# Performance work log

Hardware: AMD Instinct MI355X
Metric: run time of the kernel (lower is better)

Reference implementation:

```python
import jax, jax.numpy as jnp
import numpy as np


def _pyramid(x2, k):
    # AdaptiveAvgPool2d(k) with H,W divisible by k == block mean, then nearest upsample back
    B, C, H, W = x2.shape
    p = x2.reshape(B, C, k, H // k, k, W // k).mean(axis=(3, 5))  # [B,C,k,k]
    return jnp.repeat(jnp.repeat(p, H // k, axis=2), W // k, axis=3)  # [B,C,H,W]


def setup_inputs() -> dict:
    key = jax.random.key(0)
    ks = jax.random.split(key, 8)
    B, C, H, W = 32, 256, 32, 32
    x1 = jax.random.normal(ks[0], (B, C, H, W), jnp.float32)
    x2 = jax.random.normal(ks[1], (B, C, H, W), jnp.float32)
    # 1x1 conv weights (kaiming-ish scale), stored as [out,in]
    Wq = jax.random.normal(ks[2], (C // 2, C), jnp.float32) * (1.0 / np.sqrt(C))
    bq = jnp.zeros((C // 2,), jnp.float32)
    Wk = jax.random.normal(ks[3], (C // 2, 4 * C), jnp.float32) * (1.0 / np.sqrt(4 * C))
    bk = jnp.zeros((C // 2,), jnp.float32)
    Wv = jax.random.normal(ks[4], (C, C), jnp.float32) * (1.0 / np.sqrt(C))
    bv = jnp.zeros((C,), jnp.float32)
    return {"x1": x1, "x2": x2, "Wq": Wq, "bq": bq, "Wk": Wk, "bk": bk, "Wv": Wv, "bv": bv}


def reference(x1, x2, Wq, bq, Wk, bk, Wv, bv):
    B, C, H, W = x1.shape
    HW = H * W
    # pyramid pool at scales 1,2,4, upsampled and concatenated with x2 -> [B,4C,H,W]
    x2p = jnp.concatenate([x2] + [_pyramid(x2, k) for k in (1, 2, 4)], axis=1)
    # 1x1 convs as channel contractions
    q = (jnp.einsum('oc,bchw->bohw', Wq, x1) + bq[None, :, None, None]).reshape(B, C // 2, HW)
    k = (jnp.einsum('oc,bchw->bohw', Wk, x2p) + bk[None, :, None, None]).reshape(B, C // 2, HW)
    v = (jnp.einsum('oc,bchw->bohw', Wv, x2) + bv[None, :, None, None]).reshape(B, C, HW)
    query = q.transpose(0, 2, 1)                         # [B,HW,C/2]
    attn = jax.nn.softmax(jnp.einsum('bic,bcj->bij', query, k), axis=-1)  # [B,HW,HW]
    out = jnp.einsum('bcj,bij->bci', v, attn).reshape(B, C, H, W)
    return out + x1
```

## Files before the change

kernel.cpp:

```cpp
#include <hip/hip_runtime.h>


typedef __attribute__((ext_vector_type(8))) short short8;
typedef __attribute__((ext_vector_type(4))) float f32x4;

#define MFMA(a, b, c) __builtin_amdgcn_mfma_f32_16x16x32_bf16((a), (b), (c), 0, 0, 0)

#define GLOAD16(gp, lp)                                                        \
    __builtin_amdgcn_global_load_lds(                                          \
        (const __attribute__((address_space(1))) unsigned int*)(gp),           \
        (__attribute__((address_space(3))) unsigned int*)(lp), 16, 0, 0)

__device__ __forceinline__ unsigned short f2bf(float f) {
    unsigned u = __builtin_bit_cast(unsigned, f);
    u = (u + 0x7FFFu + ((u >> 16) & 1u)) >> 16;
    return (unsigned short)u;
}

__device__ __forceinline__ short8 ld8(const unsigned short* p) {
    return *reinterpret_cast<const short8*>(p);
}
__device__ __forceinline__ short8 ld8b(const void* base, int byte_off) {
    return *reinterpret_cast<const short8*>((const char*)base + byte_off);
}

__global__ __launch_bounds__(256) void wconv_kernel(const float* Wq, const float* Wk,
                                                    const float* Wv,
                                                    unsigned short* wqb, unsigned short* wkb,
                                                    unsigned short* wvb) {
    int i = blockIdx.x * 256 + threadIdx.x;
    if (i < 32768) { wqb[i] = f2bf(Wq[i]); return; }
    if (i < 163840) { wkb[i - 32768] = f2bf(Wk[i - 32768]); return; }
    wvb[i - 163840] = f2bf(Wv[i - 163840]);
}

__global__ __launch_bounds__(256) void transpose_kernel(const float* __restrict__ x,
                                                        unsigned short* __restrict__ xt) {
    __shared__ unsigned short tile[64][65];
    int b = blockIdx.z, c0 = blockIdx.y * 64, n0 = blockIdx.x * 64;
    const float* src = x + ((size_t)b * 256 + c0) * 1024 + n0;
    int tid = threadIdx.x;
#pragma unroll
    for (int it = 0; it < 16; ++it) {
        int idx = it * 256 + tid;
        int cl = idx >> 6, nl = idx & 63;
        tile[cl][nl] = f2bf(src[(size_t)cl * 1024 + nl]);
    }
    __syncthreads();
    int nl = tid >> 2, cs = (tid & 3) * 16;
    unsigned short buf[16];
#pragma unroll
    for (int j = 0; j < 16; ++j) buf[j] = tile[cs + j][nl];
    unsigned int w[8];
#pragma unroll
    for (int k = 0; k < 8; ++k) w[k] = (unsigned)buf[2 * k] | ((unsigned)buf[2 * k + 1] << 16);
    unsigned short* dst = xt + ((size_t)b * 1024 + n0 + nl) * 256 + c0 + cs;
    uint4 u0; u0.x = w[0]; u0.y = w[1]; u0.z = w[2]; u0.w = w[3];
    uint4 u1; u1.x = w[4]; u1.y = w[5]; u1.z = w[6]; u1.w = w[7];
    reinterpret_cast<uint4*>(dst)[0] = u0;
    reinterpret_cast<uint4*>(dst)[1] = u1;
}

__global__ __launch_bounds__(64) void pool_kernel(const float* __restrict__ x2,
                                                  float* __restrict__ p1,
                                                  float* __restrict__ p2,
                                                  float* __restrict__ p4) {
    int bc = blockIdx.x;
    int t = threadIdx.x;
    const float* src = x2 + (size_t)bc * 1024;
    int dh = t >> 3, dw = t & 7;
    float s[16];
#pragma unroll
    for (int r = 0; r < 16; ++r)
        s[r] = src[((r >> 2) * 8 + dh) * 32 + (r & 3) * 8 + dw];
#pragma unroll
    for (int r = 0; r < 16; ++r) {
        float v = s[r];
        v += __shfl_xor(v, 1);  v += __shfl_xor(v, 2);  v += __shfl_xor(v, 4);
        v += __shfl_xor(v, 8);  v += __shfl_xor(v, 16); v += __shfl_xor(v, 32);
        s[r] = v;
    }
    if (t == 0) {
        float sq[4];
#pragma unroll
        for (int j = 0; j < 4; ++j) {
            int jh = j >> 1, jw = j & 1;
            sq[j] = s[8 * jh + 2 * jw] + s[8 * jh + 2 * jw + 1] +
                    s[8 * jh + 4 + 2 * jw] + s[8 * jh + 4 + 2 * jw + 1];
            p2[(size_t)bc * 4 + j] = sq[j] * (1.f / 256.f);
        }
#pragma unroll
        for (int r = 0; r < 16; ++r) p4[(size_t)bc * 16 + r] = s[r] * (1.f / 64.f);
        p1[bc] = (sq[0] + sq[1] + sq[2] + sq[3]) * (1.f / 1024.f);
    }
}

__global__ __launch_bounds__(256) void kadd_kernel(const float* __restrict__ Wk,
                                                   const float* __restrict__ bk,
                                                   const float* __restrict__ p1,
                                                   const float* __restrict__ p2,
                                                   const float* __restrict__ p4,
                                                   float* __restrict__ kadd) {
    int b = blockIdx.x >> 7, o = blockIdx.x & 127;
    int tid = threadIdx.x;
    const float* wr = Wk + (size_t)o * 1024;
    int c = tid;
    size_t bc = (size_t)b * 256 + c;
    float vals[21];
    vals[0] = wr[256 + c] * p1[bc];
    float w2 = wr[512 + c], w4 = wr[768 + c];
#pragma unroll
    for (int j = 0; j < 4; ++j) vals[1 + j] = w2 * p2[bc * 4 + j];
#pragma unroll
    for (int r = 0; r < 16; ++r) vals[5 + r] = w4 * p4[bc * 16 + r];

    int lane = tid & 63, wid = tid >> 6;
    __shared__ float red[21][4];
    __shared__ float tot[21];
#pragma unroll
    for (int k = 0; k < 21; ++k) {
        float v = vals[k];
        v += __shfl_xor(v, 1);  v += __shfl_xor(v, 2);  v += __shfl_xor(v, 4);
        v += __shfl_xor(v, 8);  v += __shfl_xor(v, 16); v += __shfl_xor(v, 32);
        if (lane == 0) red[k][wid] = v;
    }
    __syncthreads();
    if (tid < 21) tot[tid] = red[tid][0] + red[tid][1] + red[tid][2] + red[tid][3];
    __syncthreads();
    if (tid < 16) {
        int r = tid;
        int rr = ((r >> 2) >> 1) * 2 + ((r & 3) >> 1);
        kadd[((size_t)(b * 128 + o)) * 16 + r] = bk[o] + tot[0] + tot[1 + rr] + tot[5 + r];
    }
}

template <int MODE>
__global__ __launch_bounds__(256) void gemm_kernel(const unsigned short* __restrict__ A0,
                                                   const unsigned short* __restrict__ B0,
                                                   unsigned short* __restrict__ out0,
                                                   const float* __restrict__ bias,
                                                   const float* __restrict__ kadd) {
    int b = blockIdx.z;
    const unsigned short* A;
    const unsigned short* Bp;
    unsigned short* out;
    int lda, ldb, ldo;
    if (MODE == 0) { A = A0 + (size_t)b * 262144; lda = 256; Bp = B0; ldb = 256;  out = out0 + (size_t)b * 131072; ldo = 128; }
    if (MODE == 1) { A = A0 + (size_t)b * 262144; lda = 256; Bp = B0; ldb = 1024; out = out0 + (size_t)b * 131072; ldo = 128; }
    if (MODE == 2) { A = A0;                      lda = 256; Bp = B0 + (size_t)b * 262144; ldb = 256; out = out0 + (size_t)b * 262144; ldo = 1024; }

    __shared__ unsigned short alds[128 * 64];
    __shared__ unsigned short blds[128 * 64];

    int tid = threadIdx.x;
    int w = tid >> 6, lane = tid & 63;
    int lrow = lane & 15, lk8 = (lane >> 4) * 8;
    int lk16b = lk8 * 2;
    int swl = (lrow & 7) << 4;
    int row0 = blockIdx.x * 128;
    int col0 = blockIdx.y * 128;
    int wr = (w >> 1) * 64, wc = (w & 1) * 64;

    int soff = w * 1024 + (lane << 4);
    int srow = soff >> 7;
    int scol = ((soff & 127) ^ ((srow & 7) << 4)) >> 1;

    f32x4 z = {0.f, 0.f, 0.f, 0.f};
    f32x4 acc[4][4];
#pragma unroll
    for (int i = 0; i < 4; ++i)
#pragma unroll
        for (int j = 0; j < 4; ++j) acc[i][j] = z;

    for (int kc = 0; kc < 256; kc += 64) {
#pragma unroll
        for (int it = 0; it < 4; ++it) {
            int row = it * 32 + srow;
            GLOAD16(A + (size_t)(row0 + row) * lda + kc + scol,
                    (char*)alds + it * 4096 + w * 1024);
            GLOAD16(Bp + (size_t)(col0 + row) * ldb + kc + scol,
                    (char*)blds + it * 4096 + w * 1024);
        }
        asm volatile("s_waitcnt vmcnt(0)" ::: "memory");
        __syncthreads();

#pragma unroll
        for (int kh = 0; kh < 2; ++kh) {
            short8 af[4], bfr[4];
#pragma unroll
            for (int i = 0; i < 4; ++i)
                af[i] = ld8b(alds, ((wr + i * 16 + lrow) << 7) + (((kh << 6) + lk16b) ^ swl));
#pragma unroll
            for (int j = 0; j < 4; ++j)
                bfr[j] = ld8b(blds, ((wc + j * 16 + lrow) << 7) + (((kh << 6) + lk16b) ^ swl));
#pragma unroll
            for (int i = 0; i < 4; ++i)
#pragma unroll
                for (int j = 0; j < 4; ++j) acc[i][j] = MFMA(af[i], bfr[j], acc[i][j]);
        }
        __syncthreads();
    }

#pragma unroll
    for (int i = 0; i < 4; ++i) {
#pragma unroll
        for (int j = 0; j < 4; ++j) {
            int col = col0 + wc + j * 16 + lrow;
#pragma unroll
            for (int r = 0; r < 4; ++r) {
                int row = row0 + wr + i * 16 + (lane >> 4) * 4 + r;
                float val = acc[i][j][r];
                if (MODE == 0) val += bias[col];
                if (MODE == 1) {
                    int h = row >> 5, ww = row & 31;
                    val += kadd[((size_t)(b * 128 + col)) * 16 + ((h >> 3) * 4 + (ww >> 3))];
                }
                if (MODE == 2) val += bias[row];
                out[(size_t)row * ldo + col] = f2bf(val);
            }
        }
    }
}

__global__ __launch_bounds__(256) void attn_kernel(const unsigned short* __restrict__ qt,
                                                   const unsigned short* __restrict__ kt,
                                                   const unsigned short* __restrict__ vv,
                                                   const float* __restrict__ x1,
                                                   float* __restrict__ out) {
    int b = blockIdx.x >> 4;
    int i0 = (blockIdx.x & 15) * 64;
    int tid = threadIdx.x;
    int w = tid >> 6, lane = tid & 63;
    int lrow = lane & 15, lk8 = (lane >> 4) * 8;
    int lk16b = lk8 * 2;
    int swl = (lrow & 7) << 4;
    int iw = i0 + w * 16;

    __shared__ unsigned short klds[64 * 128];
    __shared__ unsigned short vlds[256 * 64];
    __shared__ unsigned short plds[4][16][72];

    const unsigned short* qb = qt + ((size_t)b * 1024 + iw) * 128;
    const unsigned short* kb = kt + (size_t)b * 131072;
    const unsigned short* vb = vv + (size_t)b * 262144;

    short8 qf[4];
#pragma unroll
    for (int cc = 0; cc < 4; ++cc) qf[cc] = ld8(qb + (size_t)lrow * 128 + cc * 32 + lk8);

    int soff = w * 1024 + (lane << 4);
    int krow0 = soff >> 8;
    int kcb = soff & 255;
    int kcol = (kcb ^ ((krow0 & 7) << 4)) >> 1;
    int vrow0 = soff >> 7;
    int vcb = soff & 127;
    int vcol = (vcb ^ ((vrow0 & 7) << 4)) >> 1;

    f32x4 z = {0.f, 0.f, 0.f, 0.f};
    f32x4 oacc[16];
#pragma unroll
    for (int cb = 0; cb < 16; ++cb) oacc[cb] = z;
    float m_[4] = {-1e30f, -1e30f, -1e30f, -1e30f};
    float l_[4] = {0.f, 0.f, 0.f, 0.f};

    for (int j0 = 0; j0 < 1024; j0 += 64) {
#pragma unroll
        for (int it = 0; it < 4; ++it) {
            int row = it * 16 + krow0;
            GLOAD16(kb + (size_t)(j0 + row) * 128 + kcol,
                    (char*)klds + it * 4096 + w * 1024);
        }
#pragma unroll
        for (int it = 0; it < 8; ++it) {
            int row = it * 32 + vrow0;
            GLOAD16(vb + (size_t)row * 1024 + j0 + vcol,
                    (char*)vlds + it * 4096 + w * 1024);
        }
        asm volatile("s_waitcnt vmcnt(0)" ::: "memory");
        __syncthreads();

        f32x4 s[4];
#pragma unroll
        for (int jb = 0; jb < 4; ++jb) s[jb] = z;
#pragma unroll
        for (int jb = 0; jb < 4; ++jb) {
            int jrow = jb * 16 + lrow;
#pragma unroll
            for (int cc = 0; cc < 4; ++cc) {
                short8 kf = ld8b(klds, (jrow << 8) + (((cc << 6) + lk16b) ^ swl));
                s[jb] = MFMA(qf[cc], kf, s[jb]);
            }
        }

        float sc[4], rs[4];
#pragma unroll
        for (int r = 0; r < 4; ++r) {
            float t = fmaxf(fmaxf(s[0][r], s[1][r]), fmaxf(s[2][r], s[3][r]));
            t = fmaxf(t, __shfl_xor(t, 1));
            t = fmaxf(t, __shfl_xor(t, 2));
            t = fmaxf(t, __shfl_xor(t, 4));
            t = fmaxf(t, __shfl_xor(t, 8));
            float nm = fmaxf(m_[r], t);
            sc[r] = __expf(m_[r] - nm);
            m_[r] = nm;
            rs[r] = 0.f;
        }
#pragma unroll
        for (int jb = 0; jb < 4; ++jb)
#pragma unroll
            for (int r = 0; r < 4; ++r) {
                float p = __expf(s[jb][r] - m_[r]);
                rs[r] += p;
                plds[w][(lane >> 4) * 4 + r][jb * 16 + lrow] = f2bf(p);
            }
#pragma unroll
        for (int r = 0; r < 4; ++r) {
            float t = rs[r];
            t += __shfl_xor(t, 1);
            t += __shfl_xor(t, 2);
            t += __shfl_xor(t, 4);
            t += __shfl_xor(t, 8);
            l_[r] = l_[r] * sc[r] + t;
        }
#pragma unroll
        for (int cb = 0; cb < 16; ++cb)
#pragma unroll
            for (int r = 0; r < 4; ++r) oacc[cb][r] *= sc[r];

        short8 pa0 = ld8(&plds[w][lrow][lk8]);
        short8 pa1 = ld8(&plds[w][lrow][32 + lk8]);

#pragma unroll
        for (int cb = 0; cb < 16; ++cb) {
            int c = cb * 16 + lrow;
            short8 vf0 = ld8b(vlds, (c << 7) + (lk16b ^ swl));
            oacc[cb] = MFMA(pa0, vf0, oacc[cb]);
            short8 vf1 = ld8b(vlds, (c << 7) + ((64 + lk16b) ^ swl));
            oacc[cb] = MFMA(pa1, vf1, oacc[cb]);
        }
        __syncthreads();
    }

    float inv[4];
#pragma unroll
    for (int r = 0; r < 4; ++r) inv[r] = 1.f / l_[r];
    int ib = iw + (lane >> 4) * 4;
#pragma unroll
    for (int cb = 0; cb < 16; ++cb) {
        int c = cb * 16 + lrow;
        size_t g = ((size_t)b * 256 + c) * 1024 + ib;
        f32x4 xv = *reinterpret_cast<const f32x4*>(x1 + g);
        f32x4 res;
#pragma unroll
        for (int r = 0; r < 4; ++r) res[r] = oacc[cb][r] * inv[r] + xv[r];
        *reinterpret_cast<f32x4*>(out + g) = res;
    }
}

extern "C" void kernel_launch(void* const* d_in, const int* in_sizes, int n_in,
                              void* d_out, int out_size, void* d_ws, size_t ws_size,
                              hipStream_t stream) {
    const float* x1 = (const float*)d_in[0];
    const float* x2 = (const float*)d_in[1];
    const float* Wq = (const float*)d_in[2];
    const float* bq = (const float*)d_in[3];
    const float* Wk = (const float*)d_in[4];
    const float* bk = (const float*)d_in[5];
    const float* Wv = (const float*)d_in[6];
    const float* bv = (const float*)d_in[7];
    float* out = (float*)d_out;

    char* ws = (char*)d_ws;
    unsigned short* x1t = (unsigned short*)(ws + 0);
    unsigned short* x2t = (unsigned short*)(ws + 16777216);
    unsigned short* qt  = (unsigned short*)(ws + 33554432);
    unsigned short* kt  = (unsigned short*)(ws + 41943040);
    unsigned short* v   = (unsigned short*)(ws + 50331648);
    float* p1   = (float*)(ws + 67108864);
    float* p2   = (float*)(ws + 67141632);
    float* p4   = (float*)(ws + 67272704);
    float* kadd = (float*)(ws + 67796992);
    unsigned short* wqb = (unsigned short*)(ws + 68059136);
    unsigned short* wkb = (unsigned short*)(ws + 68124672);
    unsigned short* wvb = (unsigned short*)(ws + 68386816);

    wconv_kernel<<<896, 256, 0, stream>>>(Wq, Wk, Wv, wqb, wkb, wvb);

    transpose_kernel<<<dim3(16, 4, 32), 256, 0, stream>>>(x1, x1t);
    transpose_kernel<<<dim3(16, 4, 32), 256, 0, stream>>>(x2, x2t);

    pool_kernel<<<8192, 64, 0, stream>>>(x2, p1, p2, p4);
    kadd_kernel<<<4096, 256, 0, stream>>>(Wk, bk, p1, p2, p4, kadd);

    gemm_kernel<0><<<dim3(8, 1, 32), 256, 0, stream>>>(x1t, wqb, qt, bq, nullptr);
    gemm_kernel<1><<<dim3(8, 1, 32), 256, 0, stream>>>(x2t, wkb, kt, nullptr, kadd);
    gemm_kernel<2><<<dim3(2, 8, 32), 256, 0, stream>>>(wvb, x2t, v, bv, nullptr);

    attn_kernel<<<512, 256, 0, stream>>>(qt, kt, v, x1, out);
}
```

Before: 262.8 us.

## Fuse bf16 conversion into unified projection GEMM and pipeline K loads in attention

Drops the separate weight-conversion and transpose kernels. A single GEMM launch now reads fp32 x and W directly, converts to bf16 while staging into swizzled LDS, and covers the Q, K and V projections via a block-id dispatch. The attention kernel double-buffers K tiles with prefetch, overlaps V loads with the QK MFMAs, remaps blocks across batches, and applies a lazy softmax rescale that only fires when a row max grows by more than 8. This cuts launches and intermediate traffic, but staging through registers instead of direct global-to-LDS loads may slow the GEMM main loop.

```diff
diff --git a/kernel.cpp b/kernel.cpp
--- a/kernel.cpp
+++ b/kernel.cpp
@@ -16,49 +16,11 @@
     u = (u + 0x7FFFu + ((u >> 16) & 1u)) >> 16;
     return (unsigned short)u;
 }
-
 __device__ __forceinline__ short8 ld8(const unsigned short* p) {
     return *reinterpret_cast<const short8*>(p);
 }
 __device__ __forceinline__ short8 ld8b(const void* base, int byte_off) {
     return *reinterpret_cast<const short8*>((const char*)base + byte_off);
-}
-
-__global__ __launch_bounds__(256) void wconv_kernel(const float* Wq, const float* Wk,
-                                                    const float* Wv,
-                                                    unsigned short* wqb, unsigned short* wkb,
-                                                    unsigned short* wvb) {
-    int i = blockIdx.x * 256 + threadIdx.x;
-    if (i < 32768) { wqb[i] = f2bf(Wq[i]); return; }
-    if (i < 163840) { wkb[i - 32768] = f2bf(Wk[i - 32768]); return; }
-    wvb[i - 163840] = f2bf(Wv[i - 163840]);
-}
-
-__global__ __launch_bounds__(256) void transpose_kernel(const float* __restrict__ x,
-                                                        unsigned short* __restrict__ xt) {
-    __shared__ unsigned short tile[64][65];
-    int b = blockIdx.z, c0 = blockIdx.y * 64, n0 = blockIdx.x * 64;
-    const float* src = x + ((size_t)b * 256 + c0) * 1024 + n0;
-    int tid = threadIdx.x;
-#pragma unroll
-    for (int it = 0; it < 16; ++it) {
-        int idx = it * 256 + tid;
-        int cl = idx >> 6, nl = idx & 63;
-        tile[cl][nl] = f2bf(src[(size_t)cl * 1024 + nl]);
-    }
-    __syncthreads();
-    int nl = tid >> 2, cs = (tid & 3) * 16;
-    unsigned short buf[16];
-#pragma unroll
-    for (int j = 0; j < 16; ++j) buf[j] = tile[cs + j][nl];
-    unsigned int w[8];
-#pragma unroll
-    for (int k = 0; k < 8; ++k) w[k] = (unsigned)buf[2 * k] | ((unsigned)buf[2 * k + 1] << 16);
-    unsigned short* dst = xt + ((size_t)b * 1024 + n0 + nl) * 256 + c0 + cs;
-    uint4 u0; u0.x = w[0]; u0.y = w[1]; u0.z = w[2]; u0.w = w[3];
-    uint4 u1; u1.x = w[4]; u1.y = w[5]; u1.z = w[6]; u1.w = w[7];
-    reinterpret_cast<uint4*>(dst)[0] = u0;
-    reinterpret_cast<uint4*>(dst)[1] = u1;
 }
 
 __global__ __launch_bounds__(64) void pool_kernel(const float* __restrict__ x2,
@@ -134,36 +96,84 @@
     }
 }
 
-template <int MODE>
-__global__ __launch_bounds__(256) void gemm_kernel(const unsigned short* __restrict__ A0,
-                                                   const unsigned short* __restrict__ B0,
-                                                   unsigned short* __restrict__ out0,
-                                                   const float* __restrict__ bias,
-                                                   const float* __restrict__ kadd) {
-    int b = blockIdx.z;
-    const unsigned short* A;
-    const unsigned short* Bp;
-    unsigned short* out;
-    int lda, ldb, ldo;
-    if (MODE == 0) { A = A0 + (size_t)b * 262144; lda = 256; Bp = B0; ldb = 256;  out = out0 + (size_t)b * 131072; ldo = 128; }
-    if (MODE == 1) { A = A0 + (size_t)b * 262144; lda = 256; Bp = B0; ldb = 1024; out = out0 + (size_t)b * 131072; ldo = 128; }
-    if (MODE == 2) { A = A0;                      lda = 256; Bp = B0 + (size_t)b * 262144; ldb = 256; out = out0 + (size_t)b * 262144; ldo = 1024; }
-
+__device__ __forceinline__ void stage_x(unsigned short* lds, const float* X,
+                                        int n0, int kc, int tid) {
+    int c4 = (tid & 15) * 4;
+    int ng = tid >> 4;
+    const float* src = X + (size_t)(kc + c4) * 1024 + n0 + ng * 8;
+    float v[4][8];
+#pragma unroll
+    for (int i = 0; i < 4; ++i) {
+        f32x4 a = *reinterpret_cast<const f32x4*>(src + (size_t)i * 1024);
+        f32x4 bb = *reinterpret_cast<const f32x4*>(src + (size_t)i * 1024 + 4);
+#pragma unroll
+        for (int t = 0; t < 4; ++t) { v[i][t] = a[t]; v[i][4 + t] = bb[t]; }
+    }
+#pragma unroll
+    for (int j = 0; j < 8; ++j) {
+        int n = ng * 8 + j;
+        uint2 pk;
+        pk.x = (unsigned)f2bf(v[0][j]) | ((unsigned)f2bf(v[1][j]) << 16);
+        pk.y = (unsigned)f2bf(v[2][j]) | ((unsigned)f2bf(v[3][j]) << 16);
+        int byte = (n << 7) + (((tid & 15) * 8) ^ ((n & 7) << 4));
+        *reinterpret_cast<uint2*>((char*)lds + byte) = pk;
+    }
+}
+__device__ __forceinline__ void stage_w(unsigned short* lds, const float* W, int ldw,
+                                        int o0, int kc, int tid) {
+    int o = tid >> 1, h = tid & 1;
+    const float* src = W + (size_t)(o0 + o) * ldw + kc + h * 32;
+    float v[32];
+#pragma unroll
+    for (int q = 0; q < 8; ++q) {
+        f32x4 a = *reinterpret_cast<const f32x4*>(src + q * 4);
+#pragma unroll
+        for (int t = 0; t < 4; ++t) v[q * 4 + t] = a[t];
+    }
+    int swz = (o & 7) << 4;
+#pragma unroll
+    for (int q = 0; q < 4; ++q) {
+        uint4 pk;
+        pk.x = (unsigned)f2bf(v[q*8+0]) | ((unsigned)f2bf(v[q*8+1]) << 16);
+        pk.y = (unsigned)f2bf(v[q*8+2]) | ((unsigned)f2bf(v[q*8+3]) << 16);
+        pk.z = (unsigned)f2bf(v[q*8+4]) | ((unsigned)f2bf(v[q*8+5]) << 16);
+        pk.w = (unsigned)f2bf(v[q*8+6]) | ((unsigned)f2bf(v[q*8+7]) << 16);
+        int byte = (o << 7) + (((h * 64) + q * 16) ^ swz);
+        *reinterpret_cast<uint4*>((char*)lds + byte) = pk;
+    }
+}
+
+__global__ __launch_bounds__(256) void gemm_kernel(const float* __restrict__ x1,
+                                                   const float* __restrict__ x2,
+                                                   const float* __restrict__ Wq,
+                                                   const float* __restrict__ bq,
+                                                   const float* __restrict__ Wk,
+                                                   const float* __restrict__ Wv,
+                                                   const float* __restrict__ bv,
+                                                   const float* __restrict__ kadd,
+                                                   unsigned short* __restrict__ qt,
+                                                   unsigned short* __restrict__ kt,
+                                                   unsigned short* __restrict__ vv) {
     __shared__ unsigned short alds[128 * 64];
     __shared__ unsigned short blds[128 * 64];
 
+    int id = blockIdx.x;
+    int mode, bx, by = 0, b;
+    if (id < 256)      { mode = 0; b = id >> 3; bx = id & 7; }
+    else if (id < 512) { mode = 1; b = (id - 256) >> 3; bx = (id - 256) & 7; }
+    else               { int t = id - 512; mode = 2; b = t >> 4; bx = (t >> 3) & 1; by = t & 7; }
+
     int tid = threadIdx.x;
     int w = tid >> 6, lane = tid & 63;
-    int lrow = lane & 15, lk8 = (lane >> 4) * 8;
-    int lk16b = lk8 * 2;
+    int lrow = lane & 15, lk16b = (lane >> 4) * 16;
     int swl = (lrow & 7) << 4;
-    int row0 = blockIdx.x * 128;
-    int col0 = blockIdx.y * 128;
+    int row0 = bx * 128;
+    int col0 = (mode == 2) ? by * 128 : 0;
     int wr = (w >> 1) * 64, wc = (w & 1) * 64;
 
-    int soff = w * 1024 + (lane << 4);
-    int srow = soff >> 7;
-    int scol = ((soff & 127) ^ ((srow & 7) << 4)) >> 1;
+    const float* X = ((mode == 0) ? x1 : x2) + (size_t)b * 262144;
+    const float* Wmat = (mode == 0) ? Wq : (mode == 1) ? Wk : Wv;
+    int ldw = (mode == 1) ? 1024 : 256;
 
     f32x4 z = {0.f, 0.f, 0.f, 0.f};
     f32x4 acc[4][4];
@@ -173,15 +183,14 @@
         for (int j = 0; j < 4; ++j) acc[i][j] = z;
 
     for (int kc = 0; kc < 256; kc += 64) {
-#pragma unroll
-        for (int it = 0; it < 4; ++it) {
-            int row = it * 32 + srow;
-            GLOAD16(A + (size_t)(row0 + row) * lda + kc + scol,
-                    (char*)alds + it * 4096 + w * 1024);
-            GLOAD16(Bp + (size_t)(col0 + row) * ldb + kc + scol,
-                    (char*)blds + it * 4096 + w * 1024);
-        }
-        asm volatile("s_waitcnt vmcnt(0)" ::: "memory");
+        if (kc) __syncthreads();
+        if (mode != 2) {
+            stage_x(alds, X, row0, kc, tid);
+            stage_w(blds, Wmat, ldw, 0, kc, tid);
+        } else {
+            stage_w(alds, Wmat, ldw, row0, kc, tid);
+            stage_x(blds, X, col0, kc, tid);
+        }
         __syncthreads();
 
 #pragma unroll
@@ -198,9 +207,12 @@
 #pragma unroll
                 for (int j = 0; j < 4; ++j) acc[i][j] = MFMA(af[i], bfr[j], acc[i][j]);
         }
-        __syncthreads();
-    }
-
+    }
+
+    unsigned short* out = (mode == 0) ? qt + (size_t)b * 131072
+                        : (mode == 1) ? kt + (size_t)b * 131072
+                                      : vv + (size_t)b * 262144;
+    int ldo = (mode == 2) ? 1024 : 128;
 #pragma unroll
     for (int i = 0; i < 4; ++i) {
 #pragma unroll
@@ -210,12 +222,12 @@
             for (int r = 0; r < 4; ++r) {
                 int row = row0 + wr + i * 16 + (lane >> 4) * 4 + r;
                 float val = acc[i][j][r];
-                if (MODE == 0) val += bias[col];
-                if (MODE == 1) {
+                if (mode == 0) val += bq[col];
+                if (mode == 1) {
                     int h = row >> 5, ww = row & 31;
                     val += kadd[((size_t)(b * 128 + col)) * 16 + ((h >> 3) * 4 + (ww >> 3))];
                 }
-                if (MODE == 2) val += bias[row];
+                if (mode == 2) val += bv[row];
                 out[(size_t)row * ldo + col] = f2bf(val);
             }
         }
@@ -227,8 +239,10 @@
                                                    const unsigned short* __restrict__ vv,
                                                    const float* __restrict__ x1,
                                                    float* __restrict__ out) {
-    int b = blockIdx.x >> 4;
-    int i0 = (blockIdx.x & 15) * 64;
+    int bid = blockIdx.x;
+    int lid = bid >> 3;
+    int b = (bid & 7) * 4 + (lid >> 4);
+    int i0 = (lid & 15) * 64;
     int tid = threadIdx.x;
     int w = tid >> 6, lane = tid & 63;
     int lrow = lane & 15, lk8 = (lane >> 4) * 8;
@@ -236,7 +250,7 @@
     int swl = (lrow & 7) << 4;
     int iw = i0 + w * 16;
 
-    __shared__ unsigned short klds[64 * 128];
+    __shared__ unsigned short klds[2][64 * 128];
     __shared__ unsigned short vlds[256 * 64];
     __shared__ unsigned short plds[4][16][72];
 
@@ -250,11 +264,9 @@
 
     int soff = w * 1024 + (lane << 4);
     int krow0 = soff >> 8;
-    int kcb = soff & 255;
-    int kcol = (kcb ^ ((krow0 & 7) << 4)) >> 1;
+    int kcol = ((soff & 255) ^ ((krow0 & 7) << 4)) >> 1;
     int vrow0 = soff >> 7;
-    int vcb = soff & 127;
-    int vcol = (vcb ^ ((vrow0 & 7) << 4)) >> 1;
+    int vcol = ((soff & 127) ^ ((vrow0 & 7) << 4)) >> 1;
 
     f32x4 z = {0.f, 0.f, 0.f, 0.f};
     f32x4 oacc[16];
@@ -263,22 +275,22 @@
     float m_[4] = {-1e30f, -1e30f, -1e30f, -1e30f};
     float l_[4] = {0.f, 0.f, 0.f, 0.f};
 
+#pragma unroll
+    for (int it = 0; it < 4; ++it)
+        GLOAD16(kb + (size_t)(it * 16 + krow0) * 128 + kcol,
+                (char*)klds + it * 4096 + w * 1024);
+
+    int cur = 0;
     for (int j0 = 0; j0 < 1024; j0 += 64) {
-#pragma unroll
-        for (int it = 0; it < 4; ++it) {
-            int row = it * 16 + krow0;
-            GLOAD16(kb + (size_t)(j0 + row) * 128 + kcol,
-                    (char*)klds + it * 4096 + w * 1024);
-        }
-#pragma unroll
-        for (int it = 0; it < 8; ++it) {
-            int row = it * 32 + vrow0;
-            GLOAD16(vb + (size_t)row * 1024 + j0 + vcol,
-                    (char*)vlds + it * 4096 + w * 1024);
-        }
         asm volatile("s_waitcnt vmcnt(0)" ::: "memory");
         __syncthreads();
 
+#pragma unroll
+        for (int it = 0; it < 8; ++it)
+            GLOAD16(vb + (size_t)(it * 32 + vrow0) * 1024 + j0 + vcol,
+                    (char*)vlds + it * 4096 + w * 1024);
+
+        const char* kbase = (const char*)klds + cur * 16384;
         f32x4 s[4];
 #pragma unroll
         for (int jb = 0; jb < 4; ++jb) s[jb] = z;
@@ -287,12 +299,18 @@
             int jrow = jb * 16 + lrow;
 #pragma unroll
             for (int cc = 0; cc < 4; ++cc) {
-                short8 kf = ld8b(klds, (jrow << 8) + (((cc << 6) + lk16b) ^ swl));
+                short8 kf = ld8b(kbase, (jrow << 8) + (((cc << 6) + lk16b) ^ swl));
                 s[jb] = MFMA(qf[cc], kf, s[jb]);
             }
         }
 
-        float sc[4], rs[4];
+        int jn = (j0 + 64) & 1023;
+#pragma unroll
+        for (int it = 0; it < 4; ++it)
+            GLOAD16(kb + (size_t)(jn + it * 16 + krow0) * 128 + kcol,
+                    (char*)klds + (cur ^ 1) * 16384 + it * 4096 + w * 1024);
+
+        float tmax[4];
 #pragma unroll
         for (int r = 0; r < 4; ++r) {
             float t = fmaxf(fmaxf(s[0][r], s[1][r]), fmaxf(s[2][r], s[3][r]));
@@ -300,11 +318,22 @@
             t = fmaxf(t, __shfl_xor(t, 2));
             t = fmaxf(t, __shfl_xor(t, 4));
             t = fmaxf(t, __shfl_xor(t, 8));
-            float nm = fmaxf(m_[r], t);
-            sc[r] = __expf(m_[r] - nm);
-            m_[r] = nm;
-            rs[r] = 0.f;
-        }
+            tmax[r] = t;
+        }
+        bool ok = (tmax[0] <= m_[0] + 8.f) && (tmax[1] <= m_[1] + 8.f) &&
+                  (tmax[2] <= m_[2] + 8.f) && (tmax[3] <= m_[3] + 8.f);
+        if (!__all(ok)) {
+#pragma unroll
+            for (int r = 0; r < 4; ++r) {
+                float nm = fmaxf(m_[r], tmax[r]);
+                float sc = __expf(m_[r] - nm);
+                m_[r] = nm;
+                l_[r] *= sc;
+#pragma unroll
+                for (int cb = 0; cb < 16; ++cb) oacc[cb][r] *= sc;
+            }
+        }
+        float rs[4] = {0.f, 0.f, 0.f, 0.f};
 #pragma unroll
         for (int jb = 0; jb < 4; ++jb)
 #pragma unroll
@@ -320,16 +349,14 @@
             t += __shfl_xor(t, 2);
             t += __shfl_xor(t, 4);
             t += __shfl_xor(t, 8);
-            l_[r] = l_[r] * sc[r] + t;
-        }
-#pragma unroll
-        for (int cb = 0; cb < 16; ++cb)
-#pragma unroll
-            for (int r = 0; r < 4; ++r) oacc[cb][r] *= sc[r];
+            l_[r] += t;
+        }
+
+        asm volatile("s_waitcnt vmcnt(4)" ::: "memory");
+        __syncthreads();
 
         short8 pa0 = ld8(&plds[w][lrow][lk8]);
         short8 pa1 = ld8(&plds[w][lrow][32 + lk8]);
-
 #pragma unroll
         for (int cb = 0; cb < 16; ++cb) {
             int c = cb * 16 + lrow;
@@ -338,8 +365,9 @@
             short8 vf1 = ld8b(vlds, (c << 7) + ((64 + lk16b) ^ swl));
             oacc[cb] = MFMA(pa1, vf1, oacc[cb]);
         }
-        __syncthreads();
-    }
+        cur ^= 1;
+    }
+    asm volatile("s_waitcnt vmcnt(0)" ::: "memory");
 
     float inv[4];
 #pragma unroll
@@ -371,30 +399,16 @@
     float* out = (float*)d_out;
 
     char* ws = (char*)d_ws;
-    unsigned short* x1t = (unsigned short*)(ws + 0);
-    unsigned short* x2t = (unsigned short*)(ws + 16777216);
-    unsigned short* qt  = (unsigned short*)(ws + 33554432);
-    unsigned short* kt  = (unsigned short*)(ws + 41943040);
-    unsigned short* v   = (unsigned short*)(ws + 50331648);
-    float* p1   = (float*)(ws + 67108864);
-    float* p2   = (float*)(ws + 67141632);
-    float* p4   = (float*)(ws + 67272704);
-    float* kadd = (float*)(ws + 67796992);
-    unsigned short* wqb = (unsigned short*)(ws + 68059136);
-    unsigned short* wkb = (unsigned short*)(ws + 68124672);
-    unsigned short* wvb = (unsigned short*)(ws + 68386816);
-
-    wconv_kernel<<<896, 256, 0, stream>>>(Wq, Wk, Wv, wqb, wkb, wvb);
-
-    transpose_kernel<<<dim3(16, 4, 32), 256, 0, stream>>>(x1, x1t);
-    transpose_kernel<<<dim3(16, 4, 32), 256, 0, stream>>>(x2, x2t);
+    unsigned short* qt = (unsigned short*)(ws + 0);
+    unsigned short* kt = (unsigned short*)(ws + 8388608);
+    unsigned short* v  = (unsigned short*)(ws + 16777216);
+    float* p1   = (float*)(ws + 33554432);
+    float* p2   = (float*)(ws + 33587200);
+    float* p4   = (float*)(ws + 33718272);
+    float* kadd = (float*)(ws + 34242560);
 
     pool_kernel<<<8192, 64, 0, stream>>>(x2, p1, p2, p4);
     kadd_kernel<<<4096, 256, 0, stream>>>(Wk, bk, p1, p2, p4, kadd);
-
-    gemm_kernel<0><<<dim3(8, 1, 32), 256, 0, stream>>>(x1t, wqb, qt, bq, nullptr);
-    gemm_kernel<1><<<dim3(8, 1, 32), 256, 0, stream>>>(x2t, wkb, kt, nullptr, kadd);
-    gemm_kernel<2><<<dim3(2, 8, 32), 256, 0, stream>>>(wvb, x2t, v, bv, nullptr);
-
+    gemm_kernel<<<1024, 256, 0, stream>>>(x1, x2, Wq, bq, Wk, Wv, bv, kadd, qt, kt, v);
     attn_kernel<<<512, 256, 0, stream>>>(qt, kt, v, x1, out);
 }
```

New measurement: 261.3 us. About the same (-0.6%).
